# Kernel tuning notes

Hardware: AMD Instinct MI355X
Metric: run time of the kernel (lower is better)

## Reference

```python
import jax, jax.numpy as jnp
import numpy as np

B, L = 2048, 200
D_FEAT = 32            # per item-feature embedding dim
E = 3 * D_FEAT         # item embedding size = 96
U = 64                 # user embedding size
HID_ATT = 36
H1, H2 = 200, 80
V_USER, V_ITEM = 50000, 1000
EPS = 1e-8


def setup_inputs() -> dict:
    key = jax.random.key(0)
    ks = jax.random.split(key, 24)
    f = jax.random.normal
    inp = {
        "user": jax.random.randint(ks[0], (B, 1), 0, V_USER),
        "item": jax.random.randint(ks[1], (B, 3), 0, V_ITEM),
        "rec_his": jax.random.randint(ks[2], (B, L, 3), 0, V_ITEM),
        # embedding tables
        "table_user": f(ks[3], (V_USER, U), dtype=jnp.float32) * 0.05,
        "table_i1": f(ks[4], (V_ITEM, D_FEAT), dtype=jnp.float32) * 0.05,
        "table_i2": f(ks[5], (V_ITEM, D_FEAT), dtype=jnp.float32) * 0.05,
        "table_i3": f(ks[6], (V_ITEM, D_FEAT), dtype=jnp.float32) * 0.05,
        # attention MLP (LocalActivationUnit): fc1 [36, 4E], fc2 [1, 36]
        "w_att1": f(ks[7], (HID_ATT, 4 * E), dtype=jnp.float32) * 0.05,
        "b_att1": jnp.zeros((HID_ATT,), jnp.float32),
        "w_att2": f(ks[8], (1, HID_ATT), dtype=jnp.float32) * 0.05,
        "b_att2": jnp.zeros((1,), jnp.float32),
        # fc_layer: [2E+U] -> 200 -> 80 -> 1, Dice (alpha, gamma, beta) per hidden layer
        "w1": f(ks[9], (H1, 2 * E + U), dtype=jnp.float32) * 0.05,
        "b1": jnp.zeros((H1,), jnp.float32),
        "a1": f(ks[10], (H1,), dtype=jnp.float32) * 0.05,
        "g1": jnp.ones((H1,), jnp.float32),
        "be1": jnp.zeros((H1,), jnp.float32),
        "w2": f(ks[11], (H2, H1), dtype=jnp.float32) * 0.05,
        "b2": jnp.zeros((H2,), jnp.float32),
        "a2": f(ks[12], (H2,), dtype=jnp.float32) * 0.05,
        "g2": jnp.ones((H2,), jnp.float32),
        "be2": jnp.zeros((H2,), jnp.float32),
        "w3": f(ks[13], (1, H2), dtype=jnp.float32) * 0.05,
        "b3": jnp.zeros((1,), jnp.float32),
    }
    return inp


def _dice(x, alpha, gamma, beta):
    # manual batch-norm over batch dim (torch.var is unbiased, ddof=1) + Dice gate
    mean = jnp.mean(x, axis=0, keepdims=True)
    var = jnp.var(x, axis=0, ddof=1, keepdims=True)
    xn = (x - mean) / jnp.sqrt(var + EPS) * gamma + beta
    p = jax.nn.sigmoid(xn)
    return alpha * (1.0 - p) * xn + p * xn


def reference(user, item, rec_his, table_user, table_i1, table_i2, table_i3,
              w_att1, b_att1, w_att2, b_att2,
              w1, b1, a1, g1, be1, w2, b2, a2, g2, be2, w3, b3):
    user_emb = table_user[user[:, 0]]                                  # [B, U]
    item_emb = jnp.concatenate(
        [table_i1[item[:, 0]], table_i2[item[:, 1]], table_i3[item[:, 2]]], axis=1)   # [B, E]
    ub = jnp.concatenate(
        [table_i1[rec_his[:, :, 0]], table_i2[rec_his[:, :, 1]], table_i3[rec_his[:, :, 2]]],
        axis=2)                                                        # [B, L, E]
    mask = rec_his[:, :, 0] == 0                                       # [B, L] True -> zero score

    q = jnp.broadcast_to(item_emb[:, None, :], ub.shape)               # [B, L, E]
    att_in = jnp.concatenate([q, ub, q - ub, q * ub], axis=-1)          # [B, L, 4E]
    h = att_in @ w_att1.T + b_att1                                     # [B, L, 36]
    score = (h @ w_att2.T + b_att2)[..., 0]                            # [B, L]
    score = jnp.where(mask, 0.0, score)
    browse = jnp.einsum('bl,ble->be', score, ub)                       # [B, E]

    feat = jnp.concatenate([item_emb, browse, user_emb], axis=-1)      # [B, 2E+U]
    x = _dice(feat @ w1.T + b1, a1, g1, be1)
    x = _dice(x @ w2.T + b2, a2, g2, be2)
    x = jax.nn.sigmoid(x @ w3.T + b3)
    return x[:, 0]
```

## Files before the change

### kernel.cpp

```cpp
#include <hip/hip_runtime.h>
#include <math.h>

namespace {

constexpr int B   = 2048;
constexpr int L   = 200;
constexpr int E   = 96;
constexpr int U   = 64;
constexpr int NA  = 36;
constexpr int H1  = 200;
constexpr int H2  = 80;
constexpr int RB  = 8;
constexpr int NBLK = B / RB;

__device__ __forceinline__ float sigf(float x) {
    return 1.0f / (1.0f + __expf(-x));
}

template <int CTRL>
__device__ __forceinline__ float dppadd(float x) {
    int v = __builtin_amdgcn_update_dpp(0, __builtin_bit_cast(int, x),
                                        CTRL, 0xf, 0xf, true);
    return x + __builtin_bit_cast(float, v);
}
__device__ __forceinline__ float grp32_sum(float p) {
    p = dppadd<0xB1>(p);
    p = dppadd<0x4E>(p);
    p = dppadd<0x141>(p);
    p = dppadd<0x140>(p);
    p += __shfl_xor(p, 16);
    return p;
}

__global__ __launch_bounds__(256) void k_attn(
    const int* __restrict__ user, const int* __restrict__ item,
    const int* __restrict__ rec,
    const float* __restrict__ tu, const float* __restrict__ t1,
    const float* __restrict__ t2, const float* __restrict__ t3,
    const float* __restrict__ w_att1, const float* __restrict__ b_att1,
    const float* __restrict__ w_att2, const float* __restrict__ b_att2,
    float* __restrict__ feat)
{
    __shared__ float s_v[292];
    __shared__ __align__(16) float s_feat[256];
    __shared__ float s_part[8][E];
    __shared__ __align__(16) int4 s_idx4[L];

    const int b = blockIdx.x, t = threadIdx.x;
    const int g = t >> 5, lane = t & 31;

    for (int j = t; j < 289; j += 256) {
        float s;
        if (j < 96) {
            s = 0.f;
            #pragma unroll
            for (int k = 0; k < NA; ++k)
                s += w_att2[k] * (w_att1[k * 384 + j] + w_att1[k * 384 + 192 + j]);
        } else if (j < 192) {
            const int e = j - 96; s = 0.f;
            #pragma unroll
            for (int k = 0; k < NA; ++k)
                s += w_att2[k] * (w_att1[k * 384 + 96 + e] - w_att1[k * 384 + 192 + e]);
        } else if (j < 288) {
            const int e = j - 192; s = 0.f;
            #pragma unroll
            for (int k = 0; k < NA; ++k)
                s += w_att2[k] * w_att1[k * 384 + 288 + e];
        } else {
            s = b_att2[0];
            #pragma unroll
            for (int k = 0; k < NA; ++k) s += w_att2[k] * b_att1[k];
        }
        s_v[j] = s;
    }

    {
        int* si = (int*)s_idx4;
        for (int i = t; i < L * 3; i += 256) {
            const int v = rec[(size_t)b * L * 3 + i];
            si[(i / 3) * 4 + (i % 3)] = v;
        }
    }
    if (t < E) {
        const int f = t >> 5, e = t & 31;
        const float* tab = (f == 0) ? t1 : ((f == 1) ? t2 : t3);
        s_feat[t] = tab[item[b * 3 + f] * 32 + e];
    }
    if (t >= 192) s_feat[t] = tu[(size_t)user[b] * U + (t - 192)];
    __syncthreads();

    const float q0 = s_feat[lane], q1 = s_feat[32 + lane], q2 = s_feat[64 + lane];
    const float wa = s_v[96 + lane]  + q0 * s_v[192 + lane];
    const float wb = s_v[128 + lane] + q1 * s_v[224 + lane];
    const float wc = s_v[160 + lane] + q2 * s_v[256 + lane];
    float cb = q0 * s_v[lane] + q1 * s_v[32 + lane] + q2 * s_v[64 + lane];
    cb = grp32_sum(cb) + s_v[288];

    float a0 = 0.f, a1v = 0.f, a2v = 0.f;
    #pragma unroll 5
    for (int i = 0; i < 25; ++i) {
        const int4 iv = s_idx4[g * 25 + i];
        const float u0 = t1[iv.x * 32 + lane];
        const float u1 = t2[iv.y * 32 + lane];
        const float u2 = t3[iv.z * 32 + lane];
        float p = u0 * wa + u1 * wb + u2 * wc;
        p = grp32_sum(p);
        const float sc = (iv.x == 0) ? 0.f : (cb + p);
        a0 += sc * u0; a1v += sc * u1; a2v += sc * u2;
    }
    s_part[g][lane]      = a0;
    s_part[g][32 + lane] = a1v;
    s_part[g][64 + lane] = a2v;
    __syncthreads();

    if (t < E) {
        float s = 0.f;
        #pragma unroll
        for (int gg = 0; gg < 8; ++gg) s += s_part[gg][t];
        s_feat[96 + t] = s;
    }
    __syncthreads();

    feat[(size_t)b * 256 + t] = s_feat[t];
}

__global__ __launch_bounds__(256) void k_gemm1(
    const float* __restrict__ feat,
    const float* __restrict__ w1, const float* __restrict__ b1,
    float* __restrict__ y1, float* __restrict__ part1)
{
    __shared__ __align__(16) float s_f[RB * 256];
    const int t = threadIdx.x, b0 = blockIdx.x * RB;

    const float4* src = (const float4*)(feat + (size_t)b0 * 256);
    float4* dst = (float4*)s_f;
    dst[t] = src[t];
    dst[t + 256] = src[t + 256];
    __syncthreads();

    if (t < H1) {
        const float4* wr = (const float4*)(w1 + t * 256);
        float acc[RB];
        const float bj = b1[t];
        #pragma unroll
        for (int bb = 0; bb < RB; ++bb) acc[bb] = bj;
        #pragma unroll 4
        for (int k = 0; k < 64; ++k) {
            const float4 w = wr[k];
            #pragma unroll
            for (int bb = 0; bb < RB; ++bb) {
                const float4 f = ((const float4*)(s_f + bb * 256))[k];
                acc[bb] += w.x * f.x + w.y * f.y + w.z * f.z + w.w * f.w;
            }
        }
        float s1 = 0.f, s2 = 0.f;
        #pragma unroll
        for (int bb = 0; bb < RB; ++bb) {
            y1[(size_t)(b0 + bb) * H1 + t] = acc[bb];
            s1 += acc[bb]; s2 += acc[bb] * acc[bb];
        }
        part1[(size_t)blockIdx.x * 400 + t]       = s1;
        part1[(size_t)blockIdx.x * 400 + 200 + t] = s2;
    }
}

template <int NCOL, int STRIDE>
__global__ __launch_bounds__(256) void k_stats(
    const float* __restrict__ part, const float* __restrict__ g,
    const float* __restrict__ be,
    float* __restrict__ sc, float* __restrict__ sh)
{
    __shared__ float rs[256], rq[256];
    const int j = blockIdx.x, t = threadIdx.x;
    rs[t] = part[(size_t)t * STRIDE + j];
    rq[t] = part[(size_t)t * STRIDE + NCOL + j];
    __syncthreads();
    #pragma unroll
    for (int o = 128; o > 0; o >>= 1) {
        if (t < o) { rs[t] += rs[t + o]; rq[t] += rq[t + o]; }
        __syncthreads();
    }
    if (t == 0) {
        const float mean = rs[0] * (1.f / B);
        float var = (rq[0] - (float)B * mean * mean) * (1.f / (B - 1));
        var = fmaxf(var, 0.f);
        const float a = g[j] * rsqrtf(var + 1e-8f);
        sc[j] = a;
        sh[j] = be[j] - mean * a;
    }
}

__global__ __launch_bounds__(256) void k_mlp(
    const float* __restrict__ y1,
    const float* __restrict__ sc1, const float* __restrict__ sh1,
    const float* __restrict__ a1,
    const float* __restrict__ w2, const float* __restrict__ b2,
    float* __restrict__ y2, float* __restrict__ part2)
{
    __shared__ float s_c1[H1], s_h1[H1], s_al[H1];
    __shared__ __align__(16) float s_x[RB][H1];
    __shared__ float s_p1[3][H2], s_p2[3][H2];
    const int t = threadIdx.x, b0 = blockIdx.x * RB;

    if (t < H1) { s_c1[t] = sc1[t]; s_h1[t] = sh1[t]; s_al[t] = a1[t]; }
    __syncthreads();

    for (int i = t; i < RB * H1; i += 256) {
        const int j = i % H1;
        const float xn = y1[(size_t)b0 * H1 + i] * s_c1[j] + s_h1[j];
        const float p  = sigf(xn);
        s_x[i / H1][j] = xn * (p + s_al[j] * (1.f - p));
    }
    __syncthreads();

    const int j = t % H2, rg = t / H2;
    if (t < 240) {
        const int base = rg * 3;
        const int nb = (rg < 2) ? 3 : 2;
        const float4* wr = (const float4*)(w2 + j * H1);
        float acc[3];
        const float bj = b2[j];
        #pragma unroll
        for (int r = 0; r < 3; ++r) acc[r] = bj;
        #pragma unroll 2
        for (int k = 0; k < H1 / 4; ++k) {
            const float4 w = wr[k];
            for (int r = 0; r < nb; ++r) {
                const float4 x = ((const float4*)s_x[base + r])[k];
                acc[r] += w.x * x.x + w.y * x.y + w.z * x.z + w.w * x.w;
            }
        }
        float s1 = 0.f, s2 = 0.f;
        for (int r = 0; r < nb; ++r) {
            y2[(size_t)(b0 + base + r) * H2 + j] = acc[r];
            s1 += acc[r]; s2 += acc[r] * acc[r];
        }
        s_p1[rg][j] = s1; s_p2[rg][j] = s2;
    }
    __syncthreads();
    if (t < H2) {
        part2[(size_t)blockIdx.x * 160 + t]      = s_p1[0][t] + s_p1[1][t] + s_p1[2][t];
        part2[(size_t)blockIdx.x * 160 + 80 + t] = s_p2[0][t] + s_p2[1][t] + s_p2[2][t];
    }
}

__global__ __launch_bounds__(256) void k_final(
    const float* __restrict__ y2,
    const float* __restrict__ sc2, const float* __restrict__ sh2,
    const float* __restrict__ a2,
    const float* __restrict__ w3, const float* __restrict__ b3,
    float* __restrict__ out)
{
    __shared__ float s_c[H2], s_s[H2], s_aw[H2], s_w3[H2];
    const int t = threadIdx.x, b0 = blockIdx.x * RB;
    const int g = t >> 5, lane = t & 31;

    if (t < H2) {
        s_c[t] = sc2[t]; s_s[t] = sh2[t];
        s_aw[t] = a2[t]; s_w3[t] = w3[t];
    }
    __syncthreads();

    const int r = b0 + g;
    float acc = 0.f;
    #pragma unroll
    for (int jj = 0; jj < 3; ++jj) {
        const int j = lane + jj * 32;
        if (j < H2) {
            const float xn = y2[(size_t)r * H2 + j] * s_c[j] + s_s[j];
            const float p  = sigf(xn);
            acc += xn * (p + s_aw[j] * (1.f - p)) * s_w3[j];
        }
    }
    acc = grp32_sum(acc);
    if (lane == 0) out[r] = sigf(acc + b3[0]);
}

}

extern "C" void kernel_launch(void* const* d_in, const int* in_sizes, int n_in,
                              void* d_out, int out_size, void* d_ws, size_t ws_size,
                              hipStream_t stream) {
    const int*   user   = (const int*)d_in[0];
    const int*   item   = (const int*)d_in[1];
    const int*   rec    = (const int*)d_in[2];
    const float* tu     = (const float*)d_in[3];
    const float* t1     = (const float*)d_in[4];
    const float* t2     = (const float*)d_in[5];
    const float* t3     = (const float*)d_in[6];
    const float* w_att1 = (const float*)d_in[7];
    const float* b_att1 = (const float*)d_in[8];
    const float* w_att2 = (const float*)d_in[9];
    const float* b_att2 = (const float*)d_in[10];
    const float* w1     = (const float*)d_in[11];
    const float* b1     = (const float*)d_in[12];
    const float* a1     = (const float*)d_in[13];
    const float* g1     = (const float*)d_in[14];
    const float* be1    = (const float*)d_in[15];
    const float* w2     = (const float*)d_in[16];
    const float* b2     = (const float*)d_in[17];
    const float* a2     = (const float*)d_in[18];
    const float* g2     = (const float*)d_in[19];
    const float* be2    = (const float*)d_in[20];
    const float* w3     = (const float*)d_in[21];
    const float* b3     = (const float*)d_in[22];
    float* out = (float*)d_out;

    float* ws    = (float*)d_ws;
    float* part1 = ws;
    float* part2 = part1 + (size_t)NBLK * 400;
    float* sc1   = part2 + (size_t)NBLK * 160;
    float* sh1   = sc1 + 256;
    float* sc2   = sh1 + 256;
    float* sh2   = sc2 + 128;
    float* feat  = sh2 + 128;
    float* y1    = feat + (size_t)B * 256;
    float* y2    = y1 + (size_t)B * H1;

    hipLaunchKernelGGL(k_attn,  dim3(B),    dim3(256), 0, stream,
                       user, item, rec, tu, t1, t2, t3,
                       w_att1, b_att1, w_att2, b_att2, feat);
    hipLaunchKernelGGL(k_gemm1, dim3(NBLK), dim3(256), 0, stream,
                       feat, w1, b1, y1, part1);
    hipLaunchKernelGGL((k_stats<H1, 400>), dim3(H1), dim3(256), 0, stream,
                       part1, g1, be1, sc1, sh1);
    hipLaunchKernelGGL(k_mlp,   dim3(NBLK), dim3(256), 0, stream,
                       y1, sc1, sh1, a1, w2, b2, y2, part2);
    hipLaunchKernelGGL((k_stats<H2, 160>), dim3(H2), dim3(256), 0, stream,
                       part2, g2, be2, sc2, sh2);
    hipLaunchKernelGGL(k_final, dim3(NBLK), dim3(256), 0, stream,
                       y2, sc2, sh2, a2, w3, b3, out);
}
```

Measured before the change: 60.11 us.

## Fold batch-norm stats kernels into last-block reduction of producer kernels

Removes the two separate k_stats launches and instead has the last block to finish k_gemm1 and k_mlp (found with an atomic counter) reduce the per-block partial sums and compute the scale and shift. Partials are stored transposed so the final block can read each column contiguously with float4 loads and reduce it with DPP and shuffle operations. The counters are zeroed inside k_attn. This saves two kernel launches and their inter-kernel gaps, at the cost of a threadfence and an atomic in every block and a serial tail reduction done by a single block.

Result: slower. 172.6 us (+187.1%).

```diff
diff --git a/kernel.cpp b/kernel.cpp
--- a/kernel.cpp
+++ b/kernel.cpp
@@ -39,7 +39,7 @@
     const float* __restrict__ t2, const float* __restrict__ t3,
     const float* __restrict__ w_att1, const float* __restrict__ b_att1,
     const float* __restrict__ w_att2, const float* __restrict__ b_att2,
-    float* __restrict__ feat)
+    float* __restrict__ feat, int* __restrict__ ctrs)
 {
     __shared__ float s_v[292];
     __shared__ __align__(16) float s_feat[256];
@@ -48,6 +48,8 @@
 
     const int b = blockIdx.x, t = threadIdx.x;
     const int g = t >> 5, lane = t & 31;
+
+    if (b == 0 && t < 2) ctrs[t] = 0;
 
     for (int j = t; j < 289; j += 256) {
         float s;
@@ -124,12 +126,49 @@
     feat[(size_t)b * 256 + t] = s_feat[t];
 }
 
+template <int NCOL>
+__device__ __forceinline__ void lastblock_stats(
+    const float* __restrict__ partsT, const float* __restrict__ g,
+    const float* __restrict__ be, float* __restrict__ sc,
+    float* __restrict__ sh, int* __restrict__ ctr,
+    float* __restrict__ colred , int t)
+{
+    __shared__ int s_last;
+    __threadfence();
+    __syncthreads();
+    if (t == 0) s_last = (atomicAdd(ctr, 1) == NBLK - 1) ? 1 : 0;
+    __syncthreads();
+    if (!s_last) return;
+    __threadfence();
+
+    const int wv = t >> 6, ln = t & 63;
+    for (int row = wv; row < 2 * NCOL; row += 4) {
+        const float4 v = ((const float4*)(partsT + (size_t)row * NBLK))[ln];
+        float s = (v.x + v.y) + (v.z + v.w);
+        s = grp32_sum(s);
+        s += __shfl_xor(s, 32);
+        if (ln == 0) colred[row] = s;
+    }
+    __syncthreads();
+    if (t < NCOL) {
+        const float mean = colred[t] * (1.f / B);
+        float var = (colred[NCOL + t] - (float)B * mean * mean) * (1.f / (B - 1));
+        var = fmaxf(var, 0.f);
+        const float a = g[t] * rsqrtf(var + 1e-8f);
+        sc[t] = a;
+        sh[t] = be[t] - mean * a;
+    }
+}
+
 __global__ __launch_bounds__(256) void k_gemm1(
     const float* __restrict__ feat,
     const float* __restrict__ w1, const float* __restrict__ b1,
-    float* __restrict__ y1, float* __restrict__ part1)
+    const float* __restrict__ g1, const float* __restrict__ be1,
+    float* __restrict__ y1, float* __restrict__ part1t,
+    float* __restrict__ sc1, float* __restrict__ sh1, int* __restrict__ ctr)
 {
     __shared__ __align__(16) float s_f[RB * 256];
+    __shared__ float s_red[2 * H1];
     const int t = threadIdx.x, b0 = blockIdx.x * RB;
 
     const float4* src = (const float4*)(feat + (size_t)b0 * 256);
@@ -159,35 +198,11 @@
             y1[(size_t)(b0 + bb) * H1 + t] = acc[bb];
             s1 += acc[bb]; s2 += acc[bb] * acc[bb];
         }
-        part1[(size_t)blockIdx.x * 400 + t]       = s1;
-        part1[(size_t)blockIdx.x * 400 + 200 + t] = s2;
-    }
-}
-
-template <int NCOL, int STRIDE>
-__global__ __launch_bounds__(256) void k_stats(
-    const float* __restrict__ part, const float* __restrict__ g,
-    const float* __restrict__ be,
-    float* __restrict__ sc, float* __restrict__ sh)
-{
-    __shared__ float rs[256], rq[256];
-    const int j = blockIdx.x, t = threadIdx.x;
-    rs[t] = part[(size_t)t * STRIDE + j];
-    rq[t] = part[(size_t)t * STRIDE + NCOL + j];
-    __syncthreads();
-    #pragma unroll
-    for (int o = 128; o > 0; o >>= 1) {
-        if (t < o) { rs[t] += rs[t + o]; rq[t] += rq[t + o]; }
-        __syncthreads();
-    }
-    if (t == 0) {
-        const float mean = rs[0] * (1.f / B);
-        float var = (rq[0] - (float)B * mean * mean) * (1.f / (B - 1));
-        var = fmaxf(var, 0.f);
-        const float a = g[j] * rsqrtf(var + 1e-8f);
-        sc[j] = a;
-        sh[j] = be[j] - mean * a;
-    }
+        part1t[(size_t)t * NBLK + blockIdx.x]        = s1;
+        part1t[(size_t)(H1 + t) * NBLK + blockIdx.x] = s2;
+    }
+
+    lastblock_stats<H1>(part1t, g1, be1, sc1, sh1, ctr, s_red, t);
 }
 
 __global__ __launch_bounds__(256) void k_mlp(
@@ -195,11 +210,14 @@
     const float* __restrict__ sc1, const float* __restrict__ sh1,
     const float* __restrict__ a1,
     const float* __restrict__ w2, const float* __restrict__ b2,
-    float* __restrict__ y2, float* __restrict__ part2)
+    const float* __restrict__ g2, const float* __restrict__ be2,
+    float* __restrict__ y2, float* __restrict__ part2t,
+    float* __restrict__ sc2, float* __restrict__ sh2, int* __restrict__ ctr)
 {
     __shared__ float s_c1[H1], s_h1[H1], s_al[H1];
     __shared__ __align__(16) float s_x[RB][H1];
     __shared__ float s_p1[3][H2], s_p2[3][H2];
+    __shared__ float s_red[2 * H2];
     const int t = threadIdx.x, b0 = blockIdx.x * RB;
 
     if (t < H1) { s_c1[t] = sc1[t]; s_h1[t] = sh1[t]; s_al[t] = a1[t]; }
@@ -239,9 +257,11 @@
     }
     __syncthreads();
     if (t < H2) {
-        part2[(size_t)blockIdx.x * 160 + t]      = s_p1[0][t] + s_p1[1][t] + s_p1[2][t];
-        part2[(size_t)blockIdx.x * 160 + 80 + t] = s_p2[0][t] + s_p2[1][t] + s_p2[2][t];
-    }
+        part2t[(size_t)t * NBLK + blockIdx.x]        = s_p1[0][t] + s_p1[1][t] + s_p1[2][t];
+        part2t[(size_t)(H2 + t) * NBLK + blockIdx.x] = s_p2[0][t] + s_p2[1][t] + s_p2[2][t];
+    }
+
+    lastblock_stats<H2>(part2t, g2, be2, sc2, sh2, ctr, s_red, t);
 }
 
 __global__ __launch_bounds__(256) void k_final(
@@ -306,28 +326,26 @@
     const float* b3     = (const float*)d_in[22];
     float* out = (float*)d_out;
 
-    float* ws    = (float*)d_ws;
-    float* part1 = ws;
-    float* part2 = part1 + (size_t)NBLK * 400;
-    float* sc1   = part2 + (size_t)NBLK * 160;
-    float* sh1   = sc1 + 256;
-    float* sc2   = sh1 + 256;
-    float* sh2   = sc2 + 128;
-    float* feat  = sh2 + 128;
-    float* y1    = feat + (size_t)B * 256;
-    float* y2    = y1 + (size_t)B * H1;
+    float* ws     = (float*)d_ws;
+    float* part1t = ws;
+    float* part2t = part1t + (size_t)2 * H1 * NBLK;
+    float* sc1    = part2t + (size_t)2 * H2 * NBLK;
+    float* sh1    = sc1 + 256;
+    float* sc2    = sh1 + 256;
+    float* sh2    = sc2 + 128;
+    int*   ctrs   = (int*)(sh2 + 128);
+    float* feat   = (float*)(ctrs + 64);
+    float* y1     = feat + (size_t)B * 256;
+    float* y2     = y1 + (size_t)B * H1;
 
     hipLaunchKernelGGL(k_attn,  dim3(B),    dim3(256), 0, stream,
                        user, item, rec, tu, t1, t2, t3,
-                       w_att1, b_att1, w_att2, b_att2, feat);
+                       w_att1, b_att1, w_att2, b_att2, feat, ctrs);
     hipLaunchKernelGGL(k_gemm1, dim3(NBLK), dim3(256), 0, stream,
-                       feat, w1, b1, y1, part1);
-    hipLaunchKernelGGL((k_stats<H1, 400>), dim3(H1), dim3(256), 0, stream,
-                       part1, g1, be1, sc1, sh1);
+                       feat, w1, b1, g1, be1, y1, part1t, sc1, sh1, ctrs);
     hipLaunchKernelGGL(k_mlp,   dim3(NBLK), dim3(256), 0, stream,
-                       y1, sc1, sh1, a1, w2, b2, y2, part2);
-    hipLaunchKernelGGL((k_stats<H2, 160>), dim3(H2), dim3(256), 0, stream,
-                       part2, g2, be2, sc2, sh2);
+                       y1, sc1, sh1, a1, w2, b2, g2, be2, y2, part2t,
+                       sc2, sh2, ctrs + 1);
     hipLaunchKernelGGL(k_final, dim3(NBLK), dim3(256), 0, stream,
                        y2, sc2, sh2, a2, w3, b3, out);
 }
```
